# Optimization experiments

Measured on AMD Instinct MI355X. Metric: run time of the kernel, lower is better.

Reference implementation:

```python
import jax, jax.numpy as jnp
import numpy as np
from jax import lax

V, D = 50000, 300          # vocab, word_embed_dim
C, K, H = 256, 3, 256      # conv out_channels, kernel_size, hidden_size
HLU, AH, NC = 512, 256, 2  # hidden_layer_units, attn_hidden, num_classes
B, QL, AL = 64, 40, 60     # batch, question len, answer len
EPS_COS, EPS_BN = 1e-6, 1e-5


def setup_inputs() -> dict:
    key = jax.random.key(0)
    ks = jax.random.split(key, 16)
    r = lambda k, shp: (0.02 * jax.random.normal(k, shp)).astype(jnp.float32)
    return {
        "question": jax.random.randint(ks[0], (B, QL), 0, V, dtype=jnp.int32),
        "answer": jax.random.randint(ks[1], (B, AL), 0, V, dtype=jnp.int32),
        "ext_feats": jnp.zeros((B, 2), jnp.float32),
        "embedding": r(ks[2], (V, D)),
        # sm_cnn (shared for question and answer)
        "sm_convW": r(ks[3], (K, D, C)), "sm_convb": jnp.zeros((C,), jnp.float32),
        "sm_fcW": r(ks[4], (C, H)), "sm_fcb": jnp.zeros((H,), jnp.float32),
        # context_cnn
        "ctx_convW": r(ks[5], (K, D, C)), "ctx_convb": jnp.zeros((C,), jnp.float32),
        "ctx_fcW": r(ks[6], (C, H)), "ctx_fcb": jnp.zeros((H,), jnp.float32),
        # cnn_attn MLP + cnn_prob
        "attnW": r(ks[7], (H + D, AH)), "attnb": jnp.zeros((AH,), jnp.float32),
        "probW": r(ks[8], (AH, 1)),
        # final_layers: Linear(3H, HLU) + BatchNorm1d
        "W1": r(ks[9], (3 * H, HLU)), "b1": jnp.zeros((HLU,), jnp.float32),
        "gamma": jnp.ones((HLU,), jnp.float32), "beta": jnp.zeros((HLU,), jnp.float32),
        # softmax head
        "W2": r(ks[10], (HLU, NC)), "b2": jnp.zeros((NC,), jnp.float32),
    }


def _simple_cnn(x, convW, convb, fcW, fcb):
    # x: [N, L, D]; full-width Kim-CNN == conv1d over time with D input channels
    y = lax.conv_general_dilated(x, convW, (1,), 'VALID',
                                 dimension_numbers=('NWC', 'WIO', 'NWC'))
    y = jax.nn.relu(y + convb)        # [N, L-K+1, C]
    y = jnp.max(y, axis=1)            # max-pool over time -> [N, C]
    return y @ fcW + fcb              # [N, H]


def reference(question, answer, ext_feats, embedding,
              sm_convW, sm_convb, sm_fcW, sm_fcb,
              ctx_convW, ctx_convb, ctx_fcW, ctx_fcb,
              attnW, attnb, probW, W1, b1, gamma, beta, W2, b2):
    sent1 = embedding[question]                    # [B, QL, D]
    sent2 = embedding[answer]                      # [B, AL, D]

    feature1 = _simple_cnn(sent1, sm_convW, sm_convb, sm_fcW, sm_fcb)   # [B, H]
    feature2 = _simple_cnn(sent2, sm_convW, sm_convb, sm_fcW, sm_fcb)   # [B, H]

    # ---- attn_context (gating_source == 'embed') ----
    nq = jnp.linalg.norm(sent1, axis=-1)           # [B, QL]
    na = jnp.linalg.norm(sent2, axis=-1)           # [B, AL]
    dots = jnp.einsum('bqd,bad->bqa', sent1, sent2)
    cos = dots / jnp.maximum(nq[:, :, None] * na[:, None, :], EPS_COS)  # [B, QL, AL]
    attn_answer = sent2[:, None, :, :] * cos[..., None]                 # [B, QL, AL, D]
    attn_answer = attn_answer.reshape(B * QL, AL, D)

    feat = _simple_cnn(attn_answer, ctx_convW, ctx_convb, ctx_fcW, ctx_fcb)  # [B*QL, H]
    qa_comb = jnp.concatenate([feat, sent1.reshape(-1, D)], axis=1)          # [B*QL, H+D]
    score = (jnp.tanh(qa_comb @ attnW + attnb) @ probW).reshape(B, QL)
    cnn_prob = jax.nn.softmax(score, axis=1)                                 # [B, QL]
    feature3 = jnp.sum(feat.reshape(B, QL, H) * cnn_prob[..., None], axis=1)  # [B, H]

    # ---- final layers ----
    feat_comb = jnp.concatenate([feature1, feature2, feature3], axis=1)  # [B, 3H]
    h = feat_comb @ W1 + b1
    mu = jnp.mean(h, axis=0)
    var = jnp.mean((h - mu) ** 2, axis=0)          # biased, BN training mode
    h = (h - mu) / jnp.sqrt(var + EPS_BN) * gamma + beta
    feat_out = jnp.tanh(h)                          # dropout = identity (p=0)

    preds = jax.nn.log_softmax(feat_out @ W2 + b2, axis=1)
    return preds, feat_out
```

## Files before the change

kernel.cpp:

```cpp
#include <hip/hip_runtime.h>
#include <math.h>

#define Bn 64
#define QLn 40
#define ALn 60
#define Dn 300
#define KS 640
#define NQ 1024
#define NA 1536

typedef __attribute__((ext_vector_type(8))) short bf16x8;
typedef __attribute__((ext_vector_type(4))) float f32x4;

__device__ __forceinline__ float bf2f(unsigned short s) {
  return __uint_as_float(((unsigned)s) << 16);
}
__device__ __forceinline__ short f2bf(float f) {
  unsigned u = __float_as_uint(f);
  unsigned r = (u + 0x7FFFu + ((u >> 16) & 1u)) >> 16;
  return (short)r;
}

__global__ __launch_bounds__(256) void k_prep(
    const int* __restrict__ qIdx, const int* __restrict__ aIdx,
    const float* __restrict__ emb,
    const float* __restrict__ smW, const float* __restrict__ ctxW,
    const float* __restrict__ attnW, const float* __restrict__ ctxfcW,
    const float* __restrict__ ctxfcb, const float* __restrict__ attnb,
    short* __restrict__ Ae1, short* __restrict__ Ae2,
    float* __restrict__ nq, float* __restrict__ na,
    short* __restrict__ BTall, float* __restrict__ Wcat, float* __restrict__ bvec,
    float* __restrict__ numb, float* __restrict__ denb,
    float* __restrict__ logits, int* __restrict__ done) {
  __shared__ float lds[4160];
  int bid = blockIdx.x, tid = threadIdx.x;
  int w = tid >> 6, lane = tid & 63;
  if (bid < 1600) {
    int row = bid * 4 + w;
    const int* idxp; short* Ae; float* nrm; int r;
    if (row < 2560) { idxp = qIdx; Ae = Ae1; nrm = nq; r = row; }
    else { idxp = aIdx; Ae = Ae2; nrm = na; r = row - 2560; }
    int tok = idxp[r];
    const float4* src = (const float4*)(emb + (size_t)tok * Dn);
    short* d = Ae + (size_t)r * KS;
    float ssq = 0.f;
    for (int i = lane; i < 80; i += 64) {
      float4 v = (i < 75) ? src[i] : make_float4(0.f, 0.f, 0.f, 0.f);
      ssq += v.x * v.x + v.y * v.y + v.z * v.z + v.w * v.w;
      short4 h4, l4v;
      h4.x = f2bf(v.x); l4v.x = f2bf(v.x - bf2f((unsigned short)h4.x));
      h4.y = f2bf(v.y); l4v.y = f2bf(v.y - bf2f((unsigned short)h4.y));
      h4.z = f2bf(v.z); l4v.z = f2bf(v.z - bf2f((unsigned short)h4.z));
      h4.w = f2bf(v.w); l4v.w = f2bf(v.w - bf2f((unsigned short)h4.w));
      *(short4*)&d[i * 4] = h4;
      *(short4*)&d[320 + i * 4] = l4v;
    }
    #pragma unroll
    for (int o = 32; o; o >>= 1) ssq += __shfl_down(ssq, o, 64);
    if (lane == 0) nrm[r] = sqrtf(ssq);
  } else if (bid < 1800) {
    int tb = bid - 1600;
    int kt = tb % 5, nt = tb / 5;
    int n0 = nt * 64;
    const float* src; int cb;
    if (n0 < 768)       { src = smW + (n0 >> 8) * 76800; cb = n0 & 255; }
    else if (n0 < 1024) { src = attnW + 65536;           cb = n0 - 768; }
    else if (n0 < 1792) { int m = n0 - 1024; src = smW + (m >> 8) * 76800; cb = m & 255; }
    else                { int m = n0 - 1792; src = ctxW + (m >> 8) * 76800; cb = m & 255; }
    float* tile = lds;
    int nn = tid & 63;
    #pragma unroll
    for (int it = 0; it < 16; ++it) {
      int kl = it * 4 + w;
      int k = kt * 64 + kl;
      tile[kl * 65 + nn] = (k < 300) ? src[(size_t)k * 256 + cb + nn] : 0.f;
    }
    __syncthreads();
    #pragma unroll
    for (int it = 0; it < 16; ++it) {
      int nloc = it * 4 + w;
      int kl = tid & 63;
      float v = tile[kl * 65 + nloc];
      int n = n0 + nloc, k = kt * 64 + kl;
      short hi = f2bf(v), lo = f2bf(v - bf2f((unsigned short)hi));
      BTall[(size_t)n * KS + k] = hi;
      BTall[(size_t)n * KS + 320 + k] = lo;
    }
  } else if (bid < 2057) {
    int k = bid - 1800;
    float* rowv = lds;
    int j = tid;
    rowv[j] = (k < 256) ? ctxfcW[(size_t)k * 256 + j] : ctxfcb[j];
    __syncthreads();
    float a0 = 0.f, a1 = 0.f, a2 = 0.f, a3 = 0.f;
    for (int m = 0; m < 256; m += 4) {
      a0 += rowv[m]     * attnW[(size_t)m * 256 + j];
      a1 += rowv[m + 1] * attnW[(size_t)(m + 1) * 256 + j];
      a2 += rowv[m + 2] * attnW[(size_t)(m + 2) * 256 + j];
      a3 += rowv[m + 3] * attnW[(size_t)(m + 3) * 256 + j];
    }
    float acc = (a0 + a1) + (a2 + a3);
    if (k < 256) {
      Wcat[(size_t)k * 512 + j] = rowv[j];
      Wcat[(size_t)k * 512 + 256 + j] = acc;
    } else {
      bvec[j] = ctxfcb[j];
      bvec[256 + j] = acc + attnb[j];
    }
  } else {
    for (int i = tid; i < Bn * 256; i += 256) numb[i] = 0.f;
    if (tid < Bn) denb[tid] = 0.f;
    if (tid < 2 * Bn) logits[tid] = 0.f;
    if (tid == 0) *done = 0;
  }
}

__device__ __forceinline__ void gl2lds16(const short* g, short* l) {
  __builtin_amdgcn_global_load_lds(
      (const __attribute__((address_space(1))) unsigned int*)g,
      (__attribute__((address_space(3))) unsigned int*)l, 16, 0, 0);
}

__global__ __launch_bounds__(256) void k_mega(
    const short* __restrict__ Ae1, const short* __restrict__ Ae2,
    const short* __restrict__ BTall, short* __restrict__ ZQb, short* __restrict__ ZAb,
    const float* __restrict__ nq, const float* __restrict__ na,
    float* __restrict__ cosb) {
  __shared__ __align__(16) short As[128 * 32];
  __shared__ __align__(16) short Bs[128 * 32];
  int tid = threadIdx.x;
  int wid = tid >> 6, lane = tid & 63;
  int l15 = lane & 15, l4 = lane >> 4;
  int bid = blockIdx.x;
  int lin = (bid & 7) * 73 + (bid >> 3);

  if (lin < 520) {
    const short *A, *BT; short* C; int bx, by, ldc;
    if (lin < 160) {
      int chunk = lin >> 4, ww = lin & 15;
      by = ww >> 1; bx = chunk * 2 + (ww & 1);
      A = Ae1; BT = BTall; C = ZQb; ldc = NQ;
    } else {
      int l2 = lin - 160;
      int chunk = l2 / 24, ww = l2 % 24;
      by = ww >> 1; bx = chunk * 2 + (ww & 1);
      A = Ae2; BT = BTall + (size_t)1024 * KS; C = ZAb; ldc = NA;
    }
    int rowBase = bx * 128, colBase = by * 128;
    int mw = wid * 32;

    f32x4 acc[2][8];
    #pragma unroll
    for (int i = 0; i < 2; ++i)
      #pragma unroll
      for (int j = 0; j < 8; ++j) acc[i][j] = (f32x4){0.f, 0.f, 0.f, 0.f};

    int rowA0 = mw + l15, rowA1 = mw + 16 + l15;
    int sA0 = (l4 ^ ((rowA0 >> 1) & 3)) << 3;
    int sA1 = (l4 ^ ((rowA1 >> 1) & 3)) << 3;

    #pragma unroll 1
    for (int g = 0; g < 3; ++g) {
      int aoff = (g == 1) ? 320 : 0;
      int boff = (g == 2) ? 320 : 0;
      #pragma unroll 1
      for (int ks = 0; ks < 10; ++ks) {
        int ka0 = aoff + ks * 32, kb0 = boff + ks * 32;
        #pragma unroll
        for (int j = 0; j < 2; ++j) {
          int idx = tid + j * 256;
          int r = idx >> 2, s = idx & 3;
          int sl = s ^ ((r >> 1) & 3);
          int chunkStart = j * 256 + wid * 64;
          gl2lds16(A + (size_t)(rowBase + r) * KS + ka0 + (sl << 3), &As[chunkStart * 8]);
          gl2lds16(BT + (size_t)(colBase + r) * KS + kb0 + (sl << 3), &Bs[chunkStart * 8]);
        }
        __syncthreads();
        bf16x8 a0 = *reinterpret_cast<const bf16x8*>(&As[rowA0 * 32 + sA0]);
        bf16x8 a1 = *reinterpret_cast<const bf16x8*>(&As[rowA1 * 32 + sA1]);
        #pragma unroll
        for (int nj = 0; nj < 8; ++nj) {
          int rb = nj * 16 + l15;
          bf16x8 bf = *reinterpret_cast<const bf16x8*>(&Bs[rb * 32 + ((l4 ^ ((rb >> 1) & 3)) << 3)]);
          acc[0][nj] = __builtin_amdgcn_mfma_f32_16x16x32_bf16(a0, bf, acc[0][nj], 0, 0, 0);
          acc[1][nj] = __builtin_amdgcn_mfma_f32_16x16x32_bf16(a1, bf, acc[1][nj], 0, 0, 0);
        }
        __syncthreads();
      }
    }
    #pragma unroll
    for (int mi = 0; mi < 2; ++mi) {
      int row0 = rowBase + mw + mi * 16 + l4 * 4;
      #pragma unroll
      for (int nj = 0; nj < 8; ++nj) {
        int col = colBase + nj * 16 + l15;
        #pragma unroll
        for (int r = 0; r < 4; ++r)
          C[(size_t)(row0 + r) * ldc + col] = f2bf(acc[mi][nj][r]);
      }
    }
  } else {
    int b = lin - 520;
    int rowBase = b * 40, colBase = b * 60;
    f32x4 cacc[4];
    #pragma unroll
    for (int nj = 0; nj < 4; ++nj) cacc[nj] = (f32x4){0.f, 0.f, 0.f, 0.f};
    int rowA = (wid << 4) + l15;
    int sA = (l4 ^ ((rowA >> 1) & 3)) << 3;

    #pragma unroll 1
    for (int g = 0; g < 3; ++g) {
      int aoff = (g == 1) ? 320 : 0;
      int boff = (g == 2) ? 320 : 0;
      #pragma unroll 1
      for (int ks = 0; ks < 10; ++ks) {
        int ka0 = aoff + ks * 32, kb0 = boff + ks * 32;
        int r = tid >> 2, s = tid & 3;
        int sl = s ^ ((r >> 1) & 3);
        int chunkStart = wid * 64;
        int gr = rowBase + r; if (gr > 2559) gr = 2559;
        int gc = colBase + r; if (gc > 3839) gc = 3839;
        gl2lds16(Ae1 + (size_t)gr * KS + ka0 + (sl << 3), &As[chunkStart * 8]);
        gl2lds16(Ae2 + (size_t)gc * KS + kb0 + (sl << 3), &Bs[chunkStart * 8]);
        __syncthreads();
        bf16x8 a0 = *reinterpret_cast<const bf16x8*>(&As[rowA * 32 + sA]);
        #pragma unroll
        for (int nj = 0; nj < 4; ++nj) {
          int rb = (nj << 4) + l15;
          bf16x8 bf = *reinterpret_cast<const bf16x8*>(&Bs[rb * 32 + ((l4 ^ ((rb >> 1) & 3)) << 3)]);
          cacc[nj] = __builtin_amdgcn_mfma_f32_16x16x32_bf16(a0, bf, cacc[nj], 0, 0, 0);
        }
        __syncthreads();
      }
    }
    int q0 = (wid << 4) + l4 * 4;
    #pragma unroll
    for (int nj = 0; nj < 4; ++nj) {
      int a = (nj << 4) + l15;
      if (a >= ALn) continue;
      float nav = na[colBase + a];
      #pragma unroll
      for (int r = 0; r < 4; ++r) {
        int qq = q0 + r;
        if (qq < QLn) {
          float den = fmaxf(nq[rowBase + qq] * nav, 1e-6f);
          cosb[(size_t)(rowBase + qq) * ALn + a] = cacc[nj][r] / den;
        }
      }
    }
  }
}

__global__ __launch_bounds__(256) void k_fcattn(
    const short* __restrict__ ZQb, const short* __restrict__ ZAb,
    const float* __restrict__ convb, const float* __restrict__ smfcW,
    const float* __restrict__ smfcb, const float* __restrict__ cosb,
    const float* __restrict__ ctxb, const float* __restrict__ Wcat,
    const float* __restrict__ bvec, const float* __restrict__ probW,
    float* __restrict__ feat_comb, float* __restrict__ numb, float* __restrict__ denb) {
  __shared__ float lds[10816];
  int bid = blockIdx.x, j = threadIdx.x;
  if (bid < 32) {
    float* xin = lds;
    float* wt  = lds + 1024;
    int r0 = bid * 4;
    float bias0 = convb[j];
    #pragma unroll
    for (int rr = 0; rr < 4; ++rr) {
      int s = r0 + rr;
      const short* zb; int L, ld;
      if (s < Bn) { zb = ZQb + (size_t)s * QLn * NQ; L = QLn; ld = NQ; }
      else        { zb = ZAb + (size_t)(s - Bn) * ALn * NA; L = ALn; ld = NA; }
      float m = 0.f;
      for (int t = 0; t <= L - 3; ++t) {
        float v = bias0 + bf2f((unsigned short)zb[t * ld + j])
                        + bf2f((unsigned short)zb[(t + 1) * ld + 256 + j])
                        + bf2f((unsigned short)zb[(t + 2) * ld + 512 + j]);
        m = fmaxf(m, v);
      }
      xin[j * 4 + rr] = m;
    }
    float acc[4];
    #pragma unroll
    for (int rr = 0; rr < 4; ++rr) acc[rr] = smfcb[j];
    for (int ph = 0; ph < 8; ++ph) {
      const float4* src = (const float4*)(smfcW + (size_t)ph * 32 * 256);
      float4* dst = (float4*)wt;
      #pragma unroll
      for (int i = 0; i < 8; ++i) dst[i * 256 + j] = src[i * 256 + j];
      __syncthreads();
      #pragma unroll
      for (int kk = 0; kk < 32; ++kk) {
        float4 x = *reinterpret_cast<const float4*>(&xin[(ph * 32 + kk) * 4]);
        float wv = wt[kk * 256 + j];
        acc[0] += x.x * wv; acc[1] += x.y * wv; acc[2] += x.z * wv; acc[3] += x.w * wv;
      }
      __syncthreads();
    }
    #pragma unroll
    for (int rr = 0; rr < 4; ++rr) {
      int row = r0 + rr;
      feat_comb[(size_t)(row & 63) * 512 + ((row >> 6) * 256) + j] = acc[rr];
    }
  } else {
    float* xin  = lds;
    float* wt   = lds + 2048;
    float* sred = lds + 10240;
    float* cl   = lds + 10304;
    int g = bid - 32;
    int b = g / 5, q0 = (g % 5) * 8;
    int rq = b * QLn + q0;
    for (int i = j; i < 8 * ALn; i += 256)
      cl[(i / ALn) * ALn + (i % ALn)] = cosb[(size_t)(rq + i / ALn) * ALn + (i % ALn)];
    __syncthreads();
    const short* zb = ZAb + (size_t)b * ALn * NA + 768;
    float biasc = ctxb[j];
    float m[8];
    #pragma unroll
    for (int rr = 0; rr < 8; ++rr) m[rr] = 0.f;
    for (int t = 0; t <= ALn - 3; ++t) {
      float v0 = bf2f((unsigned short)zb[t * NA + j]);
      float v1 = bf2f((unsigned short)zb[(t + 1) * NA + 256 + j]);
      float v2 = bf2f((unsigned short)zb[(t + 2) * NA + 512 + j]);
      #pragma unroll
      for (int rr = 0; rr < 8; ++rr) {
        float v = biasc + cl[rr * ALn + t] * v0 + cl[rr * ALn + t + 1] * v1
                        + cl[rr * ALn + t + 2] * v2;
        m[rr] = fmaxf(m[rr], v);
      }
    }
    #pragma unroll
    for (int rr = 0; rr < 8; ++rr) xin[j * 8 + rr] = m[rr];
    float hf[8], hh[8];
    float bf0 = bvec[j], bh0 = bvec[256 + j];
    #pragma unroll
    for (int rr = 0; rr < 8; ++rr) {
      hf[rr] = bf0;
      hh[rr] = bh0 + bf2f((unsigned short)ZQb[(size_t)(rq + rr) * NQ + 768 + j]);
    }
    for (int ph = 0; ph < 16; ++ph) {
      const float4* src = (const float4*)(Wcat + (size_t)ph * 16 * 512);
      float4* dst = (float4*)wt;
      #pragma unroll
      for (int i = 0; i < 8; ++i) dst[i * 256 + j] = src[i * 256 + j];
      __syncthreads();
      #pragma unroll
      for (int kk = 0; kk < 16; ++kk) {
        int k = ph * 16 + kk;
        float4 x0 = *reinterpret_cast<const float4*>(&xin[k * 8]);
        float4 x1 = *reinterpret_cast<const float4*>(&xin[k * 8 + 4]);
        float w0 = wt[kk * 512 + j], w1 = wt[kk * 512 + 256 + j];
        hf[0] += x0.x * w0; hf[1] += x0.y * w0; hf[2] += x0.z * w0; hf[3] += x0.w * w0;
        hf[4] += x1.x * w0; hf[5] += x1.y * w0; hf[6] += x1.z * w0; hf[7] += x1.w * w0;
        hh[0] += x0.x * w1; hh[1] += x0.y * w1; hh[2] += x0.z * w1; hh[3] += x0.w * w1;
        hh[4] += x1.x * w1; hh[5] += x1.y * w1; hh[6] += x1.z * w1; hh[7] += x1.w * w1;
      }
      __syncthreads();
    }
    float pw = probW[j];
    int lane = j & 63, wv = j >> 6;
    #pragma unroll
    for (int rr = 0; rr < 8; ++rr) {
      float s = tanhf(hh[rr]) * pw;
      #pragma unroll
      for (int off = 32; off; off >>= 1) s += __shfl_down(s, off, 64);
      if (lane == 0) sred[rr * 4 + wv] = s;
    }
    __syncthreads();
    float e[8], esum = 0.f, acc3 = 0.f;
    #pragma unroll
    for (int rr = 0; rr < 8; ++rr) {
      float s = sred[rr * 4] + sred[rr * 4 + 1] + sred[rr * 4 + 2] + sred[rr * 4 + 3];
      e[rr] = __expf(s);
      esum += e[rr];
      acc3 += e[rr] * hf[rr];
    }
    atomicAdd(&numb[(size_t)b * 256 + j], acc3);
    if (j == 0) atomicAdd(&denb[b], esum);
  }
}

__global__ __launch_bounds__(256) void k_w1bn(
    const float* __restrict__ feat_comb, const float* __restrict__ numb,
    const float* __restrict__ denb, const float* __restrict__ W1,
    const float* __restrict__ b1, const float* __restrict__ gamma,
    const float* __restrict__ beta, const float* __restrict__ W2,
    const float* __restrict__ b2, float* __restrict__ feat_out,
    float* __restrict__ preds, float* __restrict__ logits, int* __restrict__ done) {
  int j0 = blockIdx.x * 8;
  int tid = threadIdx.x;
  __shared__ float wl[768][12];
  __shared__ float hb[64][8];
  __shared__ int lastflag;
  for (int it = 0; it < 24; ++it) {
    int idx = tid + it * 256;
    int k = idx >> 3, jj = idx & 7;
    wl[k][jj] = W1[(size_t)k * 512 + j0 + jj];
  }
  __syncthreads();
  int n = tid >> 2, p = tid & 3;
  float acc1[8] = {0.f, 0.f, 0.f, 0.f, 0.f, 0.f, 0.f, 0.f};
  float acc2[8] = {0.f, 0.f, 0.f, 0.f, 0.f, 0.f, 0.f, 0.f};
  const float* frow = feat_comb + (size_t)n * 512 + p;
  for (int i = 0; i < 128; ++i) {
    float v = frow[i * 4];
    int k = p + i * 4;
    float4 w0 = *reinterpret_cast<const float4*>(&wl[k][0]);
    float4 w1v = *reinterpret_cast<const float4*>(&wl[k][4]);
    acc1[0] += v * w0.x; acc1[1] += v * w0.y; acc1[2] += v * w0.z; acc1[3] += v * w0.w;
    acc1[4] += v * w1v.x; acc1[5] += v * w1v.y; acc1[6] += v * w1v.z; acc1[7] += v * w1v.w;
  }
  const float* nrow = numb + (size_t)n * 256 + p;
  for (int i = 0; i < 64; ++i) {
    float v = nrow[i * 4];
    int k = 512 + p + i * 4;
    float4 w0 = *reinterpret_cast<const float4*>(&wl[k][0]);
    float4 w1v = *reinterpret_cast<const float4*>(&wl[k][4]);
    acc2[0] += v * w0.x; acc2[1] += v * w0.y; acc2[2] += v * w0.z; acc2[3] += v * w0.w;
    acc2[4] += v * w1v.x; acc2[5] += v * w1v.y; acc2[6] += v * w1v.z; acc2[7] += v * w1v.w;
  }
  #pragma unroll
  for (int jj = 0; jj < 8; ++jj) {
    acc1[jj] += __shfl_xor(acc1[jj], 1, 64);
    acc1[jj] += __shfl_xor(acc1[jj], 2, 64);
    acc2[jj] += __shfl_xor(acc2[jj], 1, 64);
    acc2[jj] += __shfl_xor(acc2[jj], 2, 64);
  }
  if (p == 0) {
    float rden = 1.f / denb[n];
    #pragma unroll
    for (int jj = 0; jj < 8; ++jj) hb[n][jj] = acc1[jj] + rden * acc2[jj] + b1[j0 + jj];
  }
  __syncthreads();
  if (tid < 64) {
    float l0p = 0.f, l1p = 0.f;
    #pragma unroll
    for (int jj = 0; jj < 8; ++jj) {
      float v = hb[tid][jj];
      float s = v;
      #pragma unroll
      for (int off = 32; off; off >>= 1) s += __shfl_xor(s, off, 64);
      float mu = s * (1.f / 64.f);
      float d = v - mu;
      float q2 = d * d;
      #pragma unroll
      for (int off = 32; off; off >>= 1) q2 += __shfl_xor(q2, off, 64);
      float var = q2 * (1.f / 64.f);
      float fo = tanhf(d * rsqrtf(var + 1e-5f) * gamma[j0 + jj] + beta[j0 + jj]);
      feat_out[(size_t)tid * 512 + j0 + jj] = fo;
      l0p += fo * W2[(j0 + jj) * 2 + 0];
      l1p += fo * W2[(j0 + jj) * 2 + 1];
    }
    atomicAdd(&logits[tid * 2 + 0], l0p);
    atomicAdd(&logits[tid * 2 + 1], l1p);
  }
  __threadfence();
  __syncthreads();
  if (tid == 0) lastflag = (atomicAdd(done, 1) == gridDim.x - 1) ? 1 : 0;
  __syncthreads();
  if (lastflag && tid < 64) {
    __threadfence();
    float l0 = atomicAdd(&logits[tid * 2 + 0], 0.f) + b2[0];
    float l1 = atomicAdd(&logits[tid * 2 + 1], 0.f) + b2[1];
    float mx = fmaxf(l0, l1);
    float lse = mx + logf(__expf(l0 - mx) + __expf(l1 - mx));
    preds[tid * 2 + 0] = l0 - lse;
    preds[tid * 2 + 1] = l1 - lse;
  }
}

extern "C" void kernel_launch(void* const* d_in, const int* in_sizes, int n_in,
                              void* d_out, int out_size, void* d_ws, size_t ws_size,
                              hipStream_t stream) {
  (void)in_sizes; (void)n_in; (void)out_size; (void)ws_size;
  const int*   question  = (const int*)d_in[0];
  const int*   answer    = (const int*)d_in[1];
  const float* embedding = (const float*)d_in[3];
  const float* sm_convW  = (const float*)d_in[4];
  const float* sm_convb  = (const float*)d_in[5];
  const float* sm_fcW    = (const float*)d_in[6];
  const float* sm_fcb    = (const float*)d_in[7];
  const float* ctx_convW = (const float*)d_in[8];
  const float* ctx_convb = (const float*)d_in[9];
  const float* ctx_fcW   = (const float*)d_in[10];
  const float* ctx_fcb   = (const float*)d_in[11];
  const float* attnW     = (const float*)d_in[12];
  const float* attnb     = (const float*)d_in[13];
  const float* probW     = (const float*)d_in[14];
  const float* W1        = (const float*)d_in[15];
  const float* b1        = (const float*)d_in[16];
  const float* gamma     = (const float*)d_in[17];
  const float* beta      = (const float*)d_in[18];
  const float* W2        = (const float*)d_in[19];
  const float* b2        = (const float*)d_in[20];

  float* out = (float*)d_out;
  char* base = (char*)d_ws;
  size_t off = 0;
  auto alloc = [&](size_t bytes) { char* p = base + off; off += (bytes + 255) & ~(size_t)255; return p; };

  short* Ae1   = (short*)alloc(2560ull * KS * 2);
  short* Ae2   = (short*)alloc(3840ull * KS * 2);
  short* BTall = (short*)alloc(2560ull * KS * 2);
  short* ZQb   = (short*)alloc(2560ull * NQ * 2);
  short* ZAb   = (short*)alloc(3840ull * NA * 2);
  float* nq    = (float*)alloc(2560 * 4);
  float* na    = (float*)alloc(3840 * 4);
  float* cosb  = (float*)alloc(2560ull * ALn * 4);
  float* Wcat  = (float*)alloc(256ull * 512 * 4);
  float* bvec  = (float*)alloc(512 * 4);
  float* feat_comb = (float*)alloc(64ull * 512 * 4);
  float* numb   = (float*)alloc(64ull * 256 * 4);
  float* denb   = (float*)alloc(64 * 4);
  float* logits = (float*)alloc(128 * 4);
  int*   done   = (int*)alloc(256);

  k_prep<<<2058, 256, 0, stream>>>(question, answer, embedding, sm_convW, ctx_convW,
                                   attnW, ctx_fcW, ctx_fcb, attnb,
                                   Ae1, Ae2, nq, na, BTall, Wcat, bvec,
                                   numb, denb, logits, done);
  k_mega<<<584, 256, 0, stream>>>(Ae1, Ae2, BTall, ZQb, ZAb, nq, na, cosb);
  k_fcattn<<<352, 256, 0, stream>>>(ZQb, ZAb, sm_convb, sm_fcW, sm_fcb, cosb,
                                    ctx_convb, Wcat, bvec, probW,
                                    feat_comb, numb, denb);
  k_w1bn<<<64, 256, 0, stream>>>(feat_comb, numb, denb, W1, b1, gamma, beta,
                                 W2, b2, out + 128, out, logits, done);
}
```

Baseline: 121.7 us.

## Split conv max-pooling into separate kernel with time-split halves

Moves the conv-output max-pool (both the plain question/answer CNN and the cosine-weighted context CNN) out of k_fcattn into a new k_pool kernel. Each thread now handles two channels with packed bf16 loads, and the time axis is split across two thread halves whose partial maxima are merged in k_fcattn. The aim is more parallelism and fewer serial loop iterations in the pooling stage, plus less shared memory per k_fcattn block. The cost is an extra kernel launch and a round trip of partial results through global memory; the pooled partials reuse the BTall buffer.

```diff
diff --git a/kernel.cpp b/kernel.cpp
--- a/kernel.cpp
+++ b/kernel.cpp
@@ -19,6 +19,9 @@
   unsigned u = __float_as_uint(f);
   unsigned r = (u + 0x7FFFu + ((u >> 16) & 1u)) >> 16;
   return (short)r;
+}
+__device__ __forceinline__ float2 bf2x2(unsigned int p) {
+  return make_float2(__uint_as_float(p << 16), __uint_as_float(p & 0xFFFF0000u));
 }
 
 __global__ __launch_bounds__(256) void k_prep(
@@ -251,35 +254,81 @@
   }
 }
 
+__global__ __launch_bounds__(256) void k_pool(
+    const short* __restrict__ ZQb, const short* __restrict__ ZAb,
+    const float* __restrict__ convb, const float* __restrict__ cosb,
+    const float* __restrict__ ctxb,
+    float* __restrict__ pooled_part, float* __restrict__ pctx_part) {
+  __shared__ float cl[8][ALn];
+  int bid = blockIdx.x, tid = threadIdx.x;
+  int cp = tid & 127, th = tid >> 7;
+  int c2 = cp * 2;
+  if (bid < 128) {
+    int s = bid;
+    const short* zb; int L, ld;
+    if (s < Bn) { zb = ZQb + (size_t)s * QLn * NQ; L = QLn; ld = NQ; }
+    else        { zb = ZAb + (size_t)(s - Bn) * ALn * NA; L = ALn; ld = NA; }
+    int P = L - 2;
+    int t0 = th * (P >> 1), t1 = (th ? P : (P >> 1));
+    float b0 = convb[c2], b1 = convb[c2 + 1];
+    float m0 = 0.f, m1 = 0.f;
+    for (int t = t0; t < t1; ++t) {
+      float2 v0 = bf2x2(*(const unsigned int*)&zb[t * ld + c2]);
+      float2 v1 = bf2x2(*(const unsigned int*)&zb[(t + 1) * ld + 256 + c2]);
+      float2 v2 = bf2x2(*(const unsigned int*)&zb[(t + 2) * ld + 512 + c2]);
+      m0 = fmaxf(m0, b0 + v0.x + v1.x + v2.x);
+      m1 = fmaxf(m1, b1 + v0.y + v1.y + v2.y);
+    }
+    float* dst = pooled_part + ((size_t)th * 128 + s) * 256 + c2;
+    dst[0] = m0; dst[1] = m1;
+  } else {
+    int g = bid - 128;
+    int b = g / 5, q0 = (g % 5) * 8;
+    int rq = b * QLn + q0;
+    for (int i = tid; i < 8 * ALn; i += 256)
+      cl[i / ALn][i % ALn] = cosb[(size_t)(rq + i / ALn) * ALn + (i % ALn)];
+    __syncthreads();
+    const short* zb = ZAb + (size_t)b * ALn * NA + 768;
+    float b0 = ctxb[c2], b1 = ctxb[c2 + 1];
+    float m[8][2];
+    #pragma unroll
+    for (int rr = 0; rr < 8; ++rr) { m[rr][0] = 0.f; m[rr][1] = 0.f; }
+    int t0 = th * 29;
+    for (int t = t0; t < t0 + 29; ++t) {
+      float2 v0 = bf2x2(*(const unsigned int*)&zb[t * NA + c2]);
+      float2 v1 = bf2x2(*(const unsigned int*)&zb[(t + 1) * NA + 256 + c2]);
+      float2 v2 = bf2x2(*(const unsigned int*)&zb[(t + 2) * NA + 512 + c2]);
+      #pragma unroll
+      for (int rr = 0; rr < 8; ++rr) {
+        float c0 = cl[rr][t], c1 = cl[rr][t + 1], c2v = cl[rr][t + 2];
+        m[rr][0] = fmaxf(m[rr][0], b0 + c0 * v0.x + c1 * v1.x + c2v * v2.x);
+        m[rr][1] = fmaxf(m[rr][1], b1 + c0 * v0.y + c1 * v1.y + c2v * v2.y);
+      }
+    }
+    #pragma unroll
+    for (int rr = 0; rr < 8; ++rr) {
+      float* dst = pctx_part + ((size_t)th * 2560 + rq + rr) * 256 + c2;
+      dst[0] = m[rr][0]; dst[1] = m[rr][1];
+    }
+  }
+}
+
 __global__ __launch_bounds__(256) void k_fcattn(
-    const short* __restrict__ ZQb, const short* __restrict__ ZAb,
-    const float* __restrict__ convb, const float* __restrict__ smfcW,
-    const float* __restrict__ smfcb, const float* __restrict__ cosb,
-    const float* __restrict__ ctxb, const float* __restrict__ Wcat,
+    const float* __restrict__ pooled_part, const float* __restrict__ smfcW,
+    const float* __restrict__ smfcb, const float* __restrict__ pctx_part,
+    const short* __restrict__ ZQb, const float* __restrict__ Wcat,
     const float* __restrict__ bvec, const float* __restrict__ probW,
     float* __restrict__ feat_comb, float* __restrict__ numb, float* __restrict__ denb) {
-  __shared__ float lds[10816];
+  __shared__ float lds[10304];
   int bid = blockIdx.x, j = threadIdx.x;
   if (bid < 32) {
     float* xin = lds;
     float* wt  = lds + 1024;
     int r0 = bid * 4;
-    float bias0 = convb[j];
-    #pragma unroll
-    for (int rr = 0; rr < 4; ++rr) {
-      int s = r0 + rr;
-      const short* zb; int L, ld;
-      if (s < Bn) { zb = ZQb + (size_t)s * QLn * NQ; L = QLn; ld = NQ; }
-      else        { zb = ZAb + (size_t)(s - Bn) * ALn * NA; L = ALn; ld = NA; }
-      float m = 0.f;
-      for (int t = 0; t <= L - 3; ++t) {
-        float v = bias0 + bf2f((unsigned short)zb[t * ld + j])
-                        + bf2f((unsigned short)zb[(t + 1) * ld + 256 + j])
-                        + bf2f((unsigned short)zb[(t + 2) * ld + 512 + j]);
-        m = fmaxf(m, v);
-      }
-      xin[j * 4 + rr] = m;
-    }
+    #pragma unroll
+    for (int rr = 0; rr < 4; ++rr)
+      xin[j * 4 + rr] = fmaxf(pooled_part[(size_t)(r0 + rr) * 256 + j],
+                              pooled_part[(size_t)(128 + r0 + rr) * 256 + j]);
     float acc[4];
     #pragma unroll
     for (int rr = 0; rr < 4; ++rr) acc[rr] = smfcb[j];
@@ -306,31 +355,13 @@
     float* xin  = lds;
     float* wt   = lds + 2048;
     float* sred = lds + 10240;
-    float* cl   = lds + 10304;
     int g = bid - 32;
     int b = g / 5, q0 = (g % 5) * 8;
     int rq = b * QLn + q0;
-    for (int i = j; i < 8 * ALn; i += 256)
-      cl[(i / ALn) * ALn + (i % ALn)] = cosb[(size_t)(rq + i / ALn) * ALn + (i % ALn)];
-    __syncthreads();
-    const short* zb = ZAb + (size_t)b * ALn * NA + 768;
-    float biasc = ctxb[j];
-    float m[8];
-    #pragma unroll
-    for (int rr = 0; rr < 8; ++rr) m[rr] = 0.f;
-    for (int t = 0; t <= ALn - 3; ++t) {
-      float v0 = bf2f((unsigned short)zb[t * NA + j]);
-      float v1 = bf2f((unsigned short)zb[(t + 1) * NA + 256 + j]);
-      float v2 = bf2f((unsigned short)zb[(t + 2) * NA + 512 + j]);
-      #pragma unroll
-      for (int rr = 0; rr < 8; ++rr) {
-        float v = biasc + cl[rr * ALn + t] * v0 + cl[rr * ALn + t + 1] * v1
-                        + cl[rr * ALn + t + 2] * v2;
-        m[rr] = fmaxf(m[rr], v);
-      }
-    }
-    #pragma unroll
-    for (int rr = 0; rr < 8; ++rr) xin[j * 8 + rr] = m[rr];
+    #pragma unroll
+    for (int rr = 0; rr < 8; ++rr)
+      xin[j * 8 + rr] = fmaxf(pctx_part[(size_t)(rq + rr) * 256 + j],
+                              pctx_part[(size_t)(2560 + rq + rr) * 256 + j]);
     float hf[8], hh[8];
     float bf0 = bvec[j], bh0 = bvec[256 + j];
     #pragma unroll
@@ -509,19 +540,23 @@
   float* cosb  = (float*)alloc(2560ull * ALn * 4);
   float* Wcat  = (float*)alloc(256ull * 512 * 4);
   float* bvec  = (float*)alloc(512 * 4);
+  float* pctx_part = (float*)alloc(2ull * 2560 * 256 * 4);
   float* feat_comb = (float*)alloc(64ull * 512 * 4);
   float* numb   = (float*)alloc(64ull * 256 * 4);
   float* denb   = (float*)alloc(64 * 4);
   float* logits = (float*)alloc(128 * 4);
   int*   done   = (int*)alloc(256);
+  float* pooled_part = (float*)BTall;
 
   k_prep<<<2058, 256, 0, stream>>>(question, answer, embedding, sm_convW, ctx_convW,
                                    attnW, ctx_fcW, ctx_fcb, attnb,
                                    Ae1, Ae2, nq, na, BTall, Wcat, bvec,
                                    numb, denb, logits, done);
   k_mega<<<584, 256, 0, stream>>>(Ae1, Ae2, BTall, ZQb, ZAb, nq, na, cosb);
-  k_fcattn<<<352, 256, 0, stream>>>(ZQb, ZAb, sm_convb, sm_fcW, sm_fcb, cosb,
-                                    ctx_convb, Wcat, bvec, probW,
+  k_pool<<<448, 256, 0, stream>>>(ZQb, ZAb, sm_convb, cosb, ctx_convb,
+                                  pooled_part, pctx_part);
+  k_fcattn<<<352, 256, 0, stream>>>(pooled_part, sm_fcW, sm_fcb, pctx_part,
+                                    ZQb, Wcat, bvec, probW,
                                     feat_comb, numb, denb);
   k_w1bn<<<64, 256, 0, stream>>>(feat_comb, numb, denb, W1, b1, gamma, beta,
                                  W2, b2, out + 128, out, logits, done);
```

After: 110.6 us. -9.2%, faster.
